# Performance work log

Hardware: AMD Instinct MI355X
Metric: run time of the kernel (lower is better)

## Reference

```python
import jax, jax.numpy as jnp
import numpy as np


def setup_inputs() -> dict:
    key = jax.random.key(0)
    evecs = jax.random.normal(key, (4, 1, 1024, 16), dtype=jnp.float32)
    return {"evecs": evecs}


def reference(evecs):
    # Original wraps everything in torch.set_grad_enabled(False) -> block grads.
    evecs = jax.lax.stop_gradient(evecs)
    B, C, N, K = evecs.shape
    # For each level lvl, the torch loop computes X[..., :lvl+1] @ X[..., :lvl+1]^T,
    # i.e. the cumulative sum over k of rank-1 outer products e_k e_k^T.
    # outers[b, k, c, n, m] = evecs[b, c, n, k] * evecs[b, c, m, k]
    outers = jnp.einsum('bcnk,bcmk->bkcnm', evecs, evecs)
    cube = jnp.cumsum(outers, axis=1)          # running low-rank approximations
    # torch.cat(lras, dim=1): level-major then channel -> [B, K*C, N, N]
    return cube.reshape(B, K * C, N, N)
```

## Files before the change

kernel.cpp:

```cpp
#include <hip/hip_runtime.h>


#define BB 4
#define NN 1024
#define KK 16

__global__ __launch_bounds__(256) void ExpandEvecs_75780402970966_evT(
    const float* __restrict__ ev,
    float* __restrict__ evT)
{
    const int b  = blockIdx.x >> 2;
    const int mc = blockIdx.x & 3;
    const int m  = mc * 256 + threadIdx.x;
    const float* src = ev + (size_t)(b * NN + m) * KK;
    float* dst = evT + (size_t)b * KK * NN + m;
#pragma unroll
    for (int k = 0; k < KK; ++k)
        dst[(size_t)k * NN] = src[k];
}

template <bool TRANS>
__global__ __launch_bounds__(256) void ExpandEvecs_75780402970966_kernel(
    const float* __restrict__ ev,
    const float* __restrict__ evT,
    float* __restrict__ out)
{
    const int tid = threadIdx.x;
    const int m0  = tid << 2;
    const int n   = blockIdx.x & (NN - 1);
    const int b   = blockIdx.x >> 10;

    const float* __restrict__ en = ev + (size_t)(b * NN + n) * KK;

    float4 v[KK];
    if (TRANS) {
        const float* __restrict__ eT = evT + (size_t)b * KK * NN + m0;
#pragma unroll
        for (int k = 0; k < KK; ++k)
            v[k] = *(const float4*)(eT + (size_t)k * NN);
    } else {
        float4 f[16];
        const float* base = ev + ((size_t)b * NN + m0) * KK;
#pragma unroll
        for (int i = 0; i < 16; ++i)
            f[i] = *(const float4*)(base + i * 4);
#pragma unroll
        for (int k = 0; k < KK; ++k) {
            float4 t;
            t.x = ((const float*)&f[0  + (k >> 2)])[k & 3];
            t.y = ((const float*)&f[4  + (k >> 2)])[k & 3];
            t.z = ((const float*)&f[8  + (k >> 2)])[k & 3];
            t.w = ((const float*)&f[12 + (k >> 2)])[k & 3];
            v[k] = t;
        }
    }

    {
        const float e0 = en[0];
        v[0].x *= e0; v[0].y *= e0; v[0].z *= e0; v[0].w *= e0;
    }
#pragma unroll
    for (int k = 1; k < KK; ++k) {
        const float ek = en[k];
        v[k].x = fmaf(v[k].x, ek, v[k - 1].x);
        v[k].y = fmaf(v[k].y, ek, v[k - 1].y);
        v[k].z = fmaf(v[k].z, ek, v[k - 1].z);
        v[k].w = fmaf(v[k].w, ek, v[k - 1].w);
    }

    const size_t kplane = (size_t)NN * NN;
    float* ob = out + (size_t)b * KK * kplane + (size_t)n * NN + m0;
#pragma unroll
    for (int k = 0; k < KK; ++k)
        *(float4*)(ob + (size_t)k * kplane) = v[k];
}

extern "C" void kernel_launch(void* const* d_in, const int* in_sizes, int n_in,
                              void* d_out, int out_size, void* d_ws, size_t ws_size,
                              hipStream_t stream) {
    const float* ev = (const float*)d_in[0];
    float* out = (float*)d_out;

    const size_t evT_bytes = (size_t)BB * KK * NN * sizeof(float);
    if (ws_size >= evT_bytes && d_ws != nullptr) {
        float* evT = (float*)d_ws;
        ExpandEvecs_75780402970966_evT<<<BB * 4, 256, 0, stream>>>(ev, evT);
        ExpandEvecs_75780402970966_kernel<true>
            <<<BB * NN, 256, 0, stream>>>(ev, evT, out);
    } else {
        ExpandEvecs_75780402970966_kernel<false>
            <<<BB * NN, 256, 0, stream>>>(ev, nullptr, out);
    }
}
```

Baseline: 264.5 us.

## Parallelize expansion over cumulative levels so each block writes one contiguous plane chunk

```diff
diff --git a/kernel.cpp b/kernel.cpp
--- a/kernel.cpp
+++ b/kernel.cpp
@@ -4,6 +4,8 @@
 #define BB 4
 #define NN 1024
 #define KK 16
+#define ROWS 8
+#define NCHUNK (NN / ROWS)
 
 __global__ __launch_bounds__(256) void ExpandEvecs_75780402970966_evT(
     const float* __restrict__ ev,
@@ -19,7 +21,6 @@
         dst[(size_t)k * NN] = src[k];
 }
 
-template <bool TRANS>
 __global__ __launch_bounds__(256) void ExpandEvecs_75780402970966_kernel(
     const float* __restrict__ ev,
     const float* __restrict__ evT,
@@ -27,34 +28,86 @@
 {
     const int tid = threadIdx.x;
     const int m0  = tid << 2;
-    const int n   = blockIdx.x & (NN - 1);
-    const int b   = blockIdx.x >> 10;
+    const unsigned bid = blockIdx.x;
+    const int grp = bid & (NCHUNK - 1);
+    const int bk  = bid >> 7;
+    const int k   = bk & (KK - 1);
+    const int b   = bk >> 4;
+    const int n0  = grp * ROWS;
 
-    const float* __restrict__ en = ev + (size_t)(b * NN + n) * KK;
+    const float* __restrict__ eb = ev + (size_t)b * NN * KK;
+    const float* __restrict__ eT = evT + (size_t)b * KK * NN + m0;
 
-    float4 v[KK];
-    if (TRANS) {
-        const float* __restrict__ eT = evT + (size_t)b * KK * NN + m0;
+    float acc[ROWS][4];
 #pragma unroll
-        for (int k = 0; k < KK; ++k)
-            v[k] = *(const float4*)(eT + (size_t)k * NN);
-    } else {
-        float4 f[16];
-        const float* base = ev + ((size_t)b * NN + m0) * KK;
+    for (int r = 0; r < ROWS; ++r)
 #pragma unroll
-        for (int i = 0; i < 16; ++i)
-            f[i] = *(const float4*)(base + i * 4);
+        for (int v = 0; v < 4; ++v) acc[r][v] = 0.0f;
+
 #pragma unroll
-        for (int k = 0; k < KK; ++k) {
-            float4 t;
-            t.x = ((const float*)&f[0  + (k >> 2)])[k & 3];
-            t.y = ((const float*)&f[4  + (k >> 2)])[k & 3];
-            t.z = ((const float*)&f[8  + (k >> 2)])[k & 3];
-            t.w = ((const float*)&f[12 + (k >> 2)])[k & 3];
-            v[k] = t;
+    for (int kb = 0; kb < KK / 4; ++kb) {
+        if (kb * 4 <= k) {
+            float4 em4[4];
+#pragma unroll
+            for (int jj = 0; jj < 4; ++jj)
+                em4[jj] = *(const float4*)(eT + (size_t)(kb * 4 + jj) * NN);
+
+            float4 en4[ROWS];
+#pragma unroll
+            for (int r = 0; r < ROWS; ++r)
+                en4[r] = *(const float4*)(eb + (size_t)(n0 + r) * KK + kb * 4);
+
+#pragma unroll
+            for (int jj = 0; jj < 4; ++jj) {
+                const int j = kb * 4 + jj;
+                if (j <= k) {
+#pragma unroll
+                    for (int r = 0; r < ROWS; ++r) {
+                        const float enk = ((const float*)&en4[r])[jj];
+#pragma unroll
+                        for (int v = 0; v < 4; ++v)
+                            acc[r][v] = fmaf(((const float*)&em4[jj])[v], enk,
+                                             acc[r][v]);
+                    }
+                }
+            }
         }
     }
 
+    const size_t kplane = (size_t)NN * NN;
+    float* ob = out + ((size_t)(b * KK + k)) * kplane
+                    + (size_t)n0 * NN + (size_t)m0;
+#pragma unroll
+    for (int r = 0; r < ROWS; ++r)
+        *(float4*)(ob + (size_t)r * NN) =
+            make_float4(acc[r][0], acc[r][1], acc[r][2], acc[r][3]);
+}
+
+__global__ __launch_bounds__(256) void ExpandEvecs_75780402970966_fallback(
+    const float* __restrict__ ev, float* __restrict__ out)
+{
+    const int tid = threadIdx.x;
+    const int m0  = tid << 2;
+    const int n   = blockIdx.x & (NN - 1);
+    const int b   = blockIdx.x >> 10;
+    const float* __restrict__ en = ev + (size_t)(b * NN + n) * KK;
+
+    float4 f[16];
+    const float* base = ev + ((size_t)b * NN + m0) * KK;
+#pragma unroll
+    for (int i = 0; i < 16; ++i)
+        f[i] = *(const float4*)(base + i * 4);
+
+    float4 v[KK];
+#pragma unroll
+    for (int k = 0; k < KK; ++k) {
+        float4 t;
+        t.x = ((const float*)&f[0  + (k >> 2)])[k & 3];
+        t.y = ((const float*)&f[4  + (k >> 2)])[k & 3];
+        t.z = ((const float*)&f[8  + (k >> 2)])[k & 3];
+        t.w = ((const float*)&f[12 + (k >> 2)])[k & 3];
+        v[k] = t;
+    }
     {
         const float e0 = en[0];
         v[0].x *= e0; v[0].y *= e0; v[0].z *= e0; v[0].w *= e0;
@@ -67,7 +120,6 @@
         v[k].z = fmaf(v[k].z, ek, v[k - 1].z);
         v[k].w = fmaf(v[k].w, ek, v[k - 1].w);
     }
-
     const size_t kplane = (size_t)NN * NN;
     float* ob = out + (size_t)b * KK * kplane + (size_t)n * NN + m0;
 #pragma unroll
@@ -85,10 +137,10 @@
     if (ws_size >= evT_bytes && d_ws != nullptr) {
         float* evT = (float*)d_ws;
         ExpandEvecs_75780402970966_evT<<<BB * 4, 256, 0, stream>>>(ev, evT);
-        ExpandEvecs_75780402970966_kernel<true>
-            <<<BB * NN, 256, 0, stream>>>(ev, evT, out);
+        ExpandEvecs_75780402970966_kernel
+            <<<BB * KK * NCHUNK, 256, 0, stream>>>(ev, evT, out);
     } else {
-        ExpandEvecs_75780402970966_kernel<false>
-            <<<BB * NN, 256, 0, stream>>>(ev, nullptr, out);
+        ExpandEvecs_75780402970966_fallback
+            <<<BB * NN, 256, 0, stream>>>(ev, out);
     }
 }
```

New measurement: 257.8 us. 2.5% less time.

## Process eight rows per block and use nontemporal stores for output

Applied to the files above, without the earlier changes.

```diff
diff --git a/kernel.cpp b/kernel.cpp
--- a/kernel.cpp
+++ b/kernel.cpp
@@ -4,6 +4,10 @@
 #define BB 4
 #define NN 1024
 #define KK 16
+#define RPB 8
+#define NGRP (NN / RPB)
+
+typedef float f32x4 __attribute__((ext_vector_type(4)));
 
 __global__ __launch_bounds__(256) void ExpandEvecs_75780402970966_evT(
     const float* __restrict__ ev,
@@ -19,46 +23,89 @@
         dst[(size_t)k * NN] = src[k];
 }
 
-template <bool TRANS>
-__global__ __launch_bounds__(256) void ExpandEvecs_75780402970966_kernel(
+__global__ __launch_bounds__(256, 2) void ExpandEvecs_75780402970966_kernel(
     const float* __restrict__ ev,
     const float* __restrict__ evT,
     float* __restrict__ out)
 {
     const int tid = threadIdx.x;
     const int m0  = tid << 2;
+    const int ng  = blockIdx.x & (NGRP - 1);
+    const int b   = blockIdx.x >> 7;
+    const int n0  = ng * RPB;
+
+    const float* __restrict__ eb = ev  + (size_t)b * NN * KK;
+    const float* __restrict__ eT = evT + (size_t)b * KK * NN + m0;
+
+    f32x4 em[KK];
+#pragma unroll
+    for (int k = 0; k < KK; ++k)
+        em[k] = *(const f32x4*)(eT + (size_t)k * NN);
+
+    const size_t kplane = (size_t)NN * NN;
+    float* ob0 = out + (size_t)b * KK * kplane + (size_t)n0 * NN + m0;
+
+    for (int nr = 0; nr < RPB; nr += 2) {
+        const float* __restrict__ enA = eb + (size_t)(n0 + nr) * KK;
+        f32x4 vA[KK];
+        vA[0] = em[0] * enA[0];
+#pragma unroll
+        for (int k = 1; k < KK; ++k) {
+            const float e = enA[k];
+            vA[k].x = fmaf(em[k].x, e, vA[k - 1].x);
+            vA[k].y = fmaf(em[k].y, e, vA[k - 1].y);
+            vA[k].z = fmaf(em[k].z, e, vA[k - 1].z);
+            vA[k].w = fmaf(em[k].w, e, vA[k - 1].w);
+        }
+        float* obA = ob0 + (size_t)nr * NN;
+#pragma unroll
+        for (int k = 0; k < KK; ++k)
+            __builtin_nontemporal_store(vA[k], (f32x4*)(obA + (size_t)k * kplane));
+
+        const float* __restrict__ enB = eb + (size_t)(n0 + nr + 1) * KK;
+        f32x4 vB[KK];
+        vB[0] = em[0] * enB[0];
+#pragma unroll
+        for (int k = 1; k < KK; ++k) {
+            const float e = enB[k];
+            vB[k].x = fmaf(em[k].x, e, vB[k - 1].x);
+            vB[k].y = fmaf(em[k].y, e, vB[k - 1].y);
+            vB[k].z = fmaf(em[k].z, e, vB[k - 1].z);
+            vB[k].w = fmaf(em[k].w, e, vB[k - 1].w);
+        }
+        float* obB = ob0 + (size_t)(nr + 1) * NN;
+#pragma unroll
+        for (int k = 0; k < KK; ++k)
+            __builtin_nontemporal_store(vB[k], (f32x4*)(obB + (size_t)k * kplane));
+    }
+}
+
+__global__ __launch_bounds__(256) void ExpandEvecs_75780402970966_fallback(
+    const float* __restrict__ ev, float* __restrict__ out)
+{
+    const int tid = threadIdx.x;
+    const int m0  = tid << 2;
     const int n   = blockIdx.x & (NN - 1);
     const int b   = blockIdx.x >> 10;
-
     const float* __restrict__ en = ev + (size_t)(b * NN + n) * KK;
 
-    float4 v[KK];
-    if (TRANS) {
-        const float* __restrict__ eT = evT + (size_t)b * KK * NN + m0;
+    float4 f[16];
+    const float* base = ev + ((size_t)b * NN + m0) * KK;
 #pragma unroll
-        for (int k = 0; k < KK; ++k)
-            v[k] = *(const float4*)(eT + (size_t)k * NN);
-    } else {
-        float4 f[16];
-        const float* base = ev + ((size_t)b * NN + m0) * KK;
+    for (int i = 0; i < 16; ++i)
+        f[i] = *(const float4*)(base + i * 4);
+
+    f32x4 v[KK];
 #pragma unroll
-        for (int i = 0; i < 16; ++i)
-            f[i] = *(const float4*)(base + i * 4);
-#pragma unroll
-        for (int k = 0; k < KK; ++k) {
-            float4 t;
-            t.x = ((const float*)&f[0  + (k >> 2)])[k & 3];
-            t.y = ((const float*)&f[4  + (k >> 2)])[k & 3];
-            t.z = ((const float*)&f[8  + (k >> 2)])[k & 3];
-            t.w = ((const float*)&f[12 + (k >> 2)])[k & 3];
-            v[k] = t;
-        }
+    for (int k = 0; k < KK; ++k) {
+        f32x4 t;
+        t.x = ((const float*)&f[0  + (k >> 2)])[k & 3];
+        t.y = ((const float*)&f[4  + (k >> 2)])[k & 3];
+        t.z = ((const float*)&f[8  + (k >> 2)])[k & 3];
+        t.w = ((const float*)&f[12 + (k >> 2)])[k & 3];
+        v[k] = t;
     }
-
-    {
-        const float e0 = en[0];
-        v[0].x *= e0; v[0].y *= e0; v[0].z *= e0; v[0].w *= e0;
-    }
+    v[0] *= en[0];
 #pragma unroll
     for (int k = 1; k < KK; ++k) {
         const float ek = en[k];
@@ -67,12 +114,11 @@
         v[k].z = fmaf(v[k].z, ek, v[k - 1].z);
         v[k].w = fmaf(v[k].w, ek, v[k - 1].w);
     }
-
     const size_t kplane = (size_t)NN * NN;
     float* ob = out + (size_t)b * KK * kplane + (size_t)n * NN + m0;
 #pragma unroll
     for (int k = 0; k < KK; ++k)
-        *(float4*)(ob + (size_t)k * kplane) = v[k];
+        __builtin_nontemporal_store(v[k], (f32x4*)(ob + (size_t)k * kplane));
 }
 
 extern "C" void kernel_launch(void* const* d_in, const int* in_sizes, int n_in,
@@ -85,10 +131,10 @@
     if (ws_size >= evT_bytes && d_ws != nullptr) {
         float* evT = (float*)d_ws;
         ExpandEvecs_75780402970966_evT<<<BB * 4, 256, 0, stream>>>(ev, evT);
-        ExpandEvecs_75780402970966_kernel<true>
-            <<<BB * NN, 256, 0, stream>>>(ev, evT, out);
+        ExpandEvecs_75780402970966_kernel
+            <<<BB * NGRP, 256, 0, stream>>>(ev, evT, out);
     } else {
-        ExpandEvecs_75780402970966_kernel<false>
-            <<<BB * NN, 256, 0, stream>>>(ev, nullptr, out);
+        ExpandEvecs_75780402970966_fallback
+            <<<BB * NN, 256, 0, stream>>>(ev, out);
     }
 }
```

After: 266.2 us. Within noise of the previous version (+0.6%).
